# Kernel tuning notes

Measured on AMD Instinct MI355X. Metric: run time of the kernel, lower is better.

## Reference

```python
import jax, jax.numpy as jnp
import numpy as np

N_NODES = 50000
N_EDGES = 640000
WIDTH = 128
K = 5
N_CONVS = 6  # 1 input + 4 hidden + 1 output ChebConv layers


def setup_inputs() -> dict:
    key = jax.random.key(0)
    k1, k2, k3, k4 = jax.random.split(key, 4)
    scale = 1.0 / np.sqrt(WIDTH)
    x = jax.random.normal(k1, (N_NODES, WIDTH), dtype=jnp.float32)
    edge_index = jax.random.randint(k2, (2, N_EDGES), 0, N_NODES, dtype=jnp.int64)
    conv_w = jax.random.normal(k3, (N_CONVS, K, WIDTH, WIDTH), dtype=jnp.float32) * scale
    conv_b = jnp.zeros((N_CONVS, WIDTH), dtype=jnp.float32)
    lin_w = jax.random.normal(k4, (WIDTH, 1), dtype=jnp.float32) * scale
    lin_b = jnp.zeros((1,), dtype=jnp.float32)
    return {"x": x, "edge_index": edge_index, "conv_w": conv_w,
            "conv_b": conv_b, "lin_w": lin_w, "lin_b": lin_b}


def _cheb_norm(edge_index):
    # PyG ChebConv with normalization='sym', lambda_max=2.0:
    # L_hat = 2/lambda_max * (I - D^-1/2 A D^-1/2) - I = -D^-1/2 A D^-1/2
    # (diagonal terms cancel), so per-edge weight = -d_i^-1/2 * d_j^-1/2.
    src, dst = edge_index[0], edge_index[1]
    ones = jnp.ones((edge_index.shape[1],), dtype=jnp.float32)
    deg = jax.ops.segment_sum(ones, dst, num_segments=N_NODES)
    d_inv_sqrt = jnp.where(deg > 0, jax.lax.rsqrt(jnp.maximum(deg, 1e-12)), 0.0)
    return -d_inv_sqrt[src] * d_inv_sqrt[dst]


def _propagate(x, src, dst, norm):
    # L_hat @ x via gather -> weight -> scatter-add
    msg = norm[:, None] * x[src]              # [E, C]
    return jax.ops.segment_sum(msg, dst, num_segments=N_NODES)


def _cheb_conv(x, W, b, src, dst, norm):
    # Chebyshev recurrence: T0=x, T1=Lx, Tk = 2*L*T(k-1) - T(k-2)
    Tx0 = x
    out = Tx0 @ W[0]
    Tx1 = _propagate(Tx0, src, dst, norm)
    out = out + Tx1 @ W[1]
    for k in range(2, K):
        Tx2 = 2.0 * _propagate(Tx1, src, dst, norm) - Tx0
        out = out + Tx2 @ W[k]
        Tx0, Tx1 = Tx1, Tx2
    return out + b


def reference(x, edge_index, conv_w, conv_b, lin_w, lin_b):
    src, dst = edge_index[0], edge_index[1]
    norm = _cheb_norm(edge_index)
    h = x
    # first 5 convs followed by ReLU (dropout is identity in eval mode)
    for l in range(N_CONVS - 1):
        h = _cheb_conv(h, conv_w[l], conv_b[l], src, dst, norm)
        h = jax.nn.relu(h)
    # final conv (no activation) + Linear(128, 1)
    h = _cheb_conv(h, conv_w[N_CONVS - 1], conv_b[N_CONVS - 1], src, dst, norm)
    return h @ lin_w + lin_b
```

## Files before the change

kernel.cpp:

```cpp
#include <hip/hip_runtime.h>


#define NN 50000
#define NE 640000
#define WID 128

typedef __attribute__((ext_vector_type(8))) short bf16x8;
typedef __attribute__((ext_vector_type(4))) float f32x4;

__device__ __forceinline__ unsigned short f2bf(float f) {
  union { float f; unsigned int u; } v; v.f = f;
  unsigned int r = v.u + 0x7FFF + ((v.u >> 16) & 1);
  return (unsigned short)(r >> 16);
}
__device__ __forceinline__ float bflo(unsigned int u) {
  return __uint_as_float(u << 16);
}
__device__ __forceinline__ float bfhi(unsigned int u) {
  return __uint_as_float(u & 0xffff0000u);
}


__global__ __launch_bounds__(256) void degree_kernel(const int* __restrict__ ei,
                                                     int* __restrict__ deg, int E) {
  int e = blockIdx.x * 256 + threadIdx.x;
  if (e < E) atomicAdd(&deg[ei[E + e]], 1);
}

__global__ __launch_bounds__(256) void dinv_kernel(const int* __restrict__ deg,
                                                   float* __restrict__ dinv, int n) {
  int i = blockIdx.x * 256 + threadIdx.x;
  if (i < n) {
    float d = (float)deg[i];
    dinv[i] = d > 0.0f ? rsqrtf(d) : 0.0f;
  }
}

__global__ __launch_bounds__(256) void scan1_kernel(const int* __restrict__ deg,
                                                    int* __restrict__ lex,
                                                    int* __restrict__ bsum, int n) {
  __shared__ int ws[4];
  int tid = threadIdx.x, lane = tid & 63, w = tid >> 6;
  int i = blockIdx.x * 256 + tid;
  int cnt = (i < n) ? deg[i] : 0;
  int v = cnt;
#pragma unroll
  for (int off = 1; off < 64; off <<= 1) {
    int u = __shfl_up(v, off, 64);
    if (lane >= off) v += u;
  }
  if (lane == 63) ws[w] = v;
  __syncthreads();
  int wexcl = 0;
#pragma unroll
  for (int k = 0; k < 4; ++k) wexcl += (k < w) ? ws[k] : 0;
  if (i < n) lex[i] = wexcl + v - cnt;
  if (tid == 255) bsum[blockIdx.x] = wexcl + v;
}

__global__ __launch_bounds__(256) void scan2_kernel(const int* __restrict__ bsum,
                                                    int* __restrict__ boff,
                                                    int* __restrict__ row_end, int nb) {
  __shared__ int ws[4];
  int tid = threadIdx.x, lane = tid & 63, w = tid >> 6;
  int cnt = (tid < nb) ? bsum[tid] : 0;
  int v = cnt;
#pragma unroll
  for (int off = 1; off < 64; off <<= 1) {
    int u = __shfl_up(v, off, 64);
    if (lane >= off) v += u;
  }
  if (lane == 63) ws[w] = v;
  __syncthreads();
  int wexcl = 0;
#pragma unroll
  for (int k = 0; k < 4; ++k) wexcl += (k < w) ? ws[k] : 0;
  if (tid < nb) boff[tid] = wexcl + v - cnt;
  if (tid == 255) *row_end = wexcl + v;
}

__global__ __launch_bounds__(256) void scan3_kernel(const int* __restrict__ lex,
                                                    const int* __restrict__ boff,
                                                    int* __restrict__ row_start,
                                                    int* __restrict__ fill_ptr, int n) {
  int i = blockIdx.x * 256 + threadIdx.x;
  if (i < n) {
    int rs = lex[i] + boff[blockIdx.x];
    row_start[i] = rs;
    fill_ptr[i] = rs;
  }
}

__global__ __launch_bounds__(256) void fill_kernel(const int* __restrict__ ei,
                                                   const float* __restrict__ dinv,
                                                   int* __restrict__ fill_ptr,
                                                   int2* __restrict__ csr, int E) {
  int e = blockIdx.x * 256 + threadIdx.x;
  if (e < E) {
    int s = ei[e];
    int d = ei[E + e];
    int pos = atomicAdd(&fill_ptr[d], 1);
    csr[pos] = make_int2(s, __float_as_int(-dinv[s] * dinv[d]));
  }
}

__global__ __launch_bounds__(256) void cvt_x_kernel(const float* __restrict__ x,
                                                    unsigned short* __restrict__ o, int n) {
  int i = blockIdx.x * 256 + threadIdx.x;
  if (i < n) o[i] = f2bf(x[i]);
}

__global__ __launch_bounds__(256) void cvt_w_kernel(const float* __restrict__ w,
                                                    unsigned short* __restrict__ wt, int n) {
  int i = blockIdx.x * 256 + threadIdx.x;
  if (i < n) {
    int l = i / (WID * 640);
    int r = i % (WID * 640);
    int col = r / 640;
    int k = r % 640;
    int kk = k >> 7, m = k & 127;
    wt[i] = f2bf(w[(((size_t)l * 5 + kk) * WID + m) * WID + col]);
  }
}


__global__ __launch_bounds__(256) void prop_kernel(unsigned short* __restrict__ out,
                                                   const unsigned short* __restrict__ xin,
                                                   const unsigned short* __restrict__ sub,
                                                   float scale,
                                                   const int* __restrict__ row_start,
                                                   const int2* __restrict__ csr,
                                                   int n) {
  int node = blockIdx.x * 8 + (threadIdx.x >> 5);
  if (node >= n) return;
  int t = threadIdx.x & 31;
  int s = row_start[node], e = row_start[node + 1];
  float a0 = 0.f, a1 = 0.f, a2 = 0.f, a3 = 0.f;
  for (int base = s; base < e; base += 32) {
    int cnt = min(32, e - base);
    int2 ed = (t < cnt) ? csr[base + t] : make_int2(0, 0);
    int j = 0;
    for (; j + 4 <= cnt; j += 4) {
      int s0 = __shfl(ed.x, j, 32), s1 = __shfl(ed.x, j + 1, 32);
      int s2 = __shfl(ed.x, j + 2, 32), s3 = __shfl(ed.x, j + 3, 32);
      float n0 = __int_as_float(__shfl(ed.y, j, 32));
      float n1 = __int_as_float(__shfl(ed.y, j + 1, 32));
      float n2 = __int_as_float(__shfl(ed.y, j + 2, 32));
      float n3 = __int_as_float(__shfl(ed.y, j + 3, 32));
      const uint2 v0 = *(const uint2*)(xin + (size_t)s0 * WID + t * 4);
      const uint2 v1 = *(const uint2*)(xin + (size_t)s1 * WID + t * 4);
      const uint2 v2 = *(const uint2*)(xin + (size_t)s2 * WID + t * 4);
      const uint2 v3 = *(const uint2*)(xin + (size_t)s3 * WID + t * 4);
      a0 += n0 * bflo(v0.x) + n1 * bflo(v1.x) + n2 * bflo(v2.x) + n3 * bflo(v3.x);
      a1 += n0 * bfhi(v0.x) + n1 * bfhi(v1.x) + n2 * bfhi(v2.x) + n3 * bfhi(v3.x);
      a2 += n0 * bflo(v0.y) + n1 * bflo(v1.y) + n2 * bflo(v2.y) + n3 * bflo(v3.y);
      a3 += n0 * bfhi(v0.y) + n1 * bfhi(v1.y) + n2 * bfhi(v2.y) + n3 * bfhi(v3.y);
    }
    for (; j < cnt; ++j) {
      int sj = __shfl(ed.x, j, 32);
      float nj = __int_as_float(__shfl(ed.y, j, 32));
      const uint2 v = *(const uint2*)(xin + (size_t)sj * WID + t * 4);
      a0 += nj * bflo(v.x); a1 += nj * bfhi(v.x);
      a2 += nj * bflo(v.y); a3 += nj * bfhi(v.y);
    }
  }
  size_t o = (size_t)node * WID + t * 4;
  float r0 = scale * a0, r1 = scale * a1, r2 = scale * a2, r3 = scale * a3;
  if (sub) {
    const uint2 sv = *(const uint2*)(sub + o);
    r0 -= bflo(sv.x); r1 -= bfhi(sv.x);
    r2 -= bflo(sv.y); r3 -= bfhi(sv.y);
  }
  *(ushort4*)(out + o) = make_ushort4(f2bf(r0), f2bf(r1), f2bf(r2), f2bf(r3));
}


__global__ __launch_bounds__(256) void cheb_gemm(
    const unsigned short* __restrict__ T0, const unsigned short* __restrict__ T1,
    const unsigned short* __restrict__ T2, const unsigned short* __restrict__ T3,
    const unsigned short* __restrict__ T4,
    const unsigned short* __restrict__ Wt,
    const float* __restrict__ bias,
    unsigned short* __restrict__ Hb,
    const float* __restrict__ linw, const float* __restrict__ linb,
    float* __restrict__ y, int M, int mode) {
  __shared__ unsigned short As[64][40];
  __shared__ unsigned short Bs[128][40];
  const unsigned short* chunks[5] = {T0, T1, T2, T3, T4};
  int tid = threadIdx.x;
  int wave = tid >> 6, lane = tid & 63;
  int lrow = lane & 15, quad = lane >> 4;
  int rowBase = blockIdx.x * 64;

  f32x4 acc[8];
#pragma unroll
  for (int b = 0; b < 8; ++b) acc[b] = (f32x4){0.f, 0.f, 0.f, 0.f};

  int ar = tid >> 2, akof = (tid & 3) * 8;
  int agrow = min(rowBase + ar, M - 1);
  int bc = tid >> 1, bkof = (tid & 1) * 16;

  for (int kc = 0; kc < 20; ++kc) {
    const unsigned short* ch = chunks[kc >> 2];
    const unsigned short* ap = ch + (size_t)agrow * WID + (kc & 3) * 32 + akof;
    *(int4*)(&As[ar][akof]) = *(const int4*)ap;
    const unsigned short* bp = Wt + (size_t)bc * 640 + kc * 32 + bkof;
    *(int4*)(&Bs[bc][bkof]) = *(const int4*)bp;
    *(int4*)(&Bs[bc][bkof + 8]) = *(const int4*)(bp + 8);
    __syncthreads();

    bf16x8 a = *(bf16x8*)(&As[wave * 16 + lrow][quad * 8]);
#pragma unroll
    for (int ct = 0; ct < 8; ++ct) {
      bf16x8 b = *(bf16x8*)(&Bs[ct * 16 + lrow][quad * 8]);
      acc[ct] = __builtin_amdgcn_mfma_f32_16x16x32_bf16(a, b, acc[ct], 0, 0, 0);
    }
    __syncthreads();
  }

  if (mode != 2) {
#pragma unroll
    for (int ct = 0; ct < 8; ++ct) {
      int gcol = ct * 16 + lrow;
      float bv = bias[gcol];
#pragma unroll
      for (int reg = 0; reg < 4; ++reg) {
        int grow = rowBase + wave * 16 + quad * 4 + reg;
        if (grow < M) {
          float v = acc[ct][reg] + bv;
          if (mode == 1) v = fmaxf(v, 0.f);
          Hb[(size_t)grow * WID + gcol] = f2bf(v);
        }
      }
    }
  } else {
    float lwv[8], bvv[8];
#pragma unroll
    for (int ct = 0; ct < 8; ++ct) {
      int gcol = ct * 16 + lrow;
      lwv[ct] = linw[gcol];
      bvv[ct] = bias[gcol];
    }
#pragma unroll
    for (int reg = 0; reg < 4; ++reg) {
      float part = 0.f;
#pragma unroll
      for (int ct = 0; ct < 8; ++ct) part += (acc[ct][reg] + bvv[ct]) * lwv[ct];
#pragma unroll
      for (int off = 1; off < 16; off <<= 1) part += __shfl_xor(part, off, 16);
      int grow = rowBase + wave * 16 + quad * 4 + reg;
      if (lrow == 0 && grow < M) y[grow] = part + linb[0];
    }
  }
}


extern "C" void kernel_launch(void* const* d_in, const int* in_sizes, int n_in,
                              void* d_out, int out_size, void* d_ws, size_t ws_size,
                              hipStream_t stream) {
  const float* x = (const float*)d_in[0];
  const int* ei = (const int*)d_in[1];
  const float* conv_w = (const float*)d_in[2];
  const float* conv_b = (const float*)d_in[3];
  const float* lin_w = (const float*)d_in[4];
  const float* lin_b = (const float*)d_in[5];

  const int N = NN, E = NE, C = WID, L = 6;
  const int NB = (N + 255) / 256;

  char* ws = (char*)d_ws;
  size_t off = 0;
  auto alloc = [&](size_t bytes) -> void* {
    void* p = ws + off;
    off = (off + bytes + 255) & ~(size_t)255;
    return p;
  };
  int* deg = (int*)alloc((size_t)N * 4);
  float* dinv = (float*)alloc((size_t)N * 4);
  int* row_start = (int*)alloc((size_t)(N + 1) * 4);
  int* fill_ptr = (int*)alloc((size_t)N * 4);
  int* lex = (int*)alloc((size_t)N * 4);
  int* bsum = (int*)alloc((size_t)NB * 4);
  int* boff = (int*)alloc((size_t)NB * 4);
  int2* csr = (int2*)alloc((size_t)E * 8);
  unsigned short* Xbf = (unsigned short*)alloc((size_t)N * C * 2);
  unsigned short* Hb0 = (unsigned short*)alloc((size_t)N * C * 2);
  unsigned short* Hb1 = (unsigned short*)alloc((size_t)N * C * 2);
  unsigned short* T1b = (unsigned short*)alloc((size_t)N * C * 2);
  unsigned short* T2b = (unsigned short*)alloc((size_t)N * C * 2);
  unsigned short* T3b = (unsigned short*)alloc((size_t)N * C * 2);
  unsigned short* T4b = (unsigned short*)alloc((size_t)N * C * 2);
  unsigned short* Wt = (unsigned short*)alloc((size_t)L * C * 640 * 2);

  hipMemsetAsync(deg, 0, (size_t)N * 4, stream);
  degree_kernel<<<(E + 255) / 256, 256, 0, stream>>>(ei, deg, E);
  dinv_kernel<<<(N + 255) / 256, 256, 0, stream>>>(deg, dinv, N);
  scan1_kernel<<<NB, 256, 0, stream>>>(deg, lex, bsum, N);
  scan2_kernel<<<1, 256, 0, stream>>>(bsum, boff, &row_start[N], NB);
  scan3_kernel<<<NB, 256, 0, stream>>>(lex, boff, row_start, fill_ptr, N);
  fill_kernel<<<(E + 255) / 256, 256, 0, stream>>>(ei, dinv, fill_ptr, csr, E);
  cvt_x_kernel<<<(N * C + 255) / 256, 256, 0, stream>>>(x, Xbf, N * C);
  cvt_w_kernel<<<(L * C * 640 + 255) / 256, 256, 0, stream>>>(conv_w, Wt, L * C * 640);

  const int pg = (N + 7) / 8;
  const int gg = (N + 63) / 64;

  for (int l = 0; l < L; ++l) {
    const unsigned short* T0 = (l == 0) ? Xbf : ((l & 1) ? Hb0 : Hb1);
    unsigned short* Hb = (l & 1) ? Hb1 : Hb0;
    int mode = (l < L - 1) ? 1 : 2;

    prop_kernel<<<pg, 256, 0, stream>>>(T1b, T0, nullptr, 1.0f, row_start, csr, N);
    prop_kernel<<<pg, 256, 0, stream>>>(T2b, T1b, T0, 2.0f, row_start, csr, N);
    prop_kernel<<<pg, 256, 0, stream>>>(T3b, T2b, T1b, 2.0f, row_start, csr, N);
    prop_kernel<<<pg, 256, 0, stream>>>(T4b, T3b, T2b, 2.0f, row_start, csr, N);
    cheb_gemm<<<gg, 256, 0, stream>>>(T0, T1b, T2b, T3b, T4b,
                                      Wt + (size_t)l * C * 640, conv_b + (size_t)l * C,
                                      Hb, lin_w, lin_b, (float*)d_out, N, mode);
  }
}
```

Before: 972.2 us.

## Widen SpMM gather to 16-byte loads and register-prefetch GEMM tiles

The propagation kernel now assigns 16 lanes per node, each loading 8 bf16 values (uint4) per neighbor row instead of 4. This halves the shuffle and loop overhead per edge and processes twice as many nodes per block. The Chebyshev GEMM now prefetches the next K-chunk of A and B into registers while the current chunk is in shared memory, hiding global load latency behind MFMA work. The cost is more registers per thread, and the 16-lane shuffle width reduces edge-batch parallelism for high-degree nodes.

```diff
diff --git a/kernel.cpp b/kernel.cpp
--- a/kernel.cpp
+++ b/kernel.cpp
@@ -12,6 +12,9 @@
   union { float f; unsigned int u; } v; v.f = f;
   unsigned int r = v.u + 0x7FFF + ((v.u >> 16) & 1);
   return (unsigned short)(r >> 16);
+}
+__device__ __forceinline__ unsigned int pack2(float lo, float hi) {
+  return (unsigned int)f2bf(lo) | ((unsigned int)f2bf(hi) << 16);
 }
 __device__ __forceinline__ float bflo(unsigned int u) {
   return __uint_as_float(u << 16);
@@ -131,47 +134,60 @@
                                                    const int* __restrict__ row_start,
                                                    const int2* __restrict__ csr,
                                                    int n) {
-  int node = blockIdx.x * 8 + (threadIdx.x >> 5);
+  int node = blockIdx.x * 16 + (threadIdx.x >> 4);
   if (node >= n) return;
-  int t = threadIdx.x & 31;
+  int t = threadIdx.x & 15;
   int s = row_start[node], e = row_start[node + 1];
   float a0 = 0.f, a1 = 0.f, a2 = 0.f, a3 = 0.f;
-  for (int base = s; base < e; base += 32) {
-    int cnt = min(32, e - base);
+  float a4 = 0.f, a5 = 0.f, a6 = 0.f, a7 = 0.f;
+  for (int base = s; base < e; base += 16) {
+    int cnt = min(16, e - base);
     int2 ed = (t < cnt) ? csr[base + t] : make_int2(0, 0);
     int j = 0;
     for (; j + 4 <= cnt; j += 4) {
-      int s0 = __shfl(ed.x, j, 32), s1 = __shfl(ed.x, j + 1, 32);
-      int s2 = __shfl(ed.x, j + 2, 32), s3 = __shfl(ed.x, j + 3, 32);
-      float n0 = __int_as_float(__shfl(ed.y, j, 32));
-      float n1 = __int_as_float(__shfl(ed.y, j + 1, 32));
-      float n2 = __int_as_float(__shfl(ed.y, j + 2, 32));
-      float n3 = __int_as_float(__shfl(ed.y, j + 3, 32));
-      const uint2 v0 = *(const uint2*)(xin + (size_t)s0 * WID + t * 4);
-      const uint2 v1 = *(const uint2*)(xin + (size_t)s1 * WID + t * 4);
-      const uint2 v2 = *(const uint2*)(xin + (size_t)s2 * WID + t * 4);
-      const uint2 v3 = *(const uint2*)(xin + (size_t)s3 * WID + t * 4);
+      int s0 = __shfl(ed.x, j, 16), s1 = __shfl(ed.x, j + 1, 16);
+      int s2 = __shfl(ed.x, j + 2, 16), s3 = __shfl(ed.x, j + 3, 16);
+      float n0 = __int_as_float(__shfl(ed.y, j, 16));
+      float n1 = __int_as_float(__shfl(ed.y, j + 1, 16));
+      float n2 = __int_as_float(__shfl(ed.y, j + 2, 16));
+      float n3 = __int_as_float(__shfl(ed.y, j + 3, 16));
+      const uint4 v0 = *(const uint4*)(xin + (size_t)s0 * WID + t * 8);
+      const uint4 v1 = *(const uint4*)(xin + (size_t)s1 * WID + t * 8);
+      const uint4 v2 = *(const uint4*)(xin + (size_t)s2 * WID + t * 8);
+      const uint4 v3 = *(const uint4*)(xin + (size_t)s3 * WID + t * 8);
       a0 += n0 * bflo(v0.x) + n1 * bflo(v1.x) + n2 * bflo(v2.x) + n3 * bflo(v3.x);
       a1 += n0 * bfhi(v0.x) + n1 * bfhi(v1.x) + n2 * bfhi(v2.x) + n3 * bfhi(v3.x);
       a2 += n0 * bflo(v0.y) + n1 * bflo(v1.y) + n2 * bflo(v2.y) + n3 * bflo(v3.y);
       a3 += n0 * bfhi(v0.y) + n1 * bfhi(v1.y) + n2 * bfhi(v2.y) + n3 * bfhi(v3.y);
+      a4 += n0 * bflo(v0.z) + n1 * bflo(v1.z) + n2 * bflo(v2.z) + n3 * bflo(v3.z);
+      a5 += n0 * bfhi(v0.z) + n1 * bfhi(v1.z) + n2 * bfhi(v2.z) + n3 * bfhi(v3.z);
+      a6 += n0 * bflo(v0.w) + n1 * bflo(v1.w) + n2 * bflo(v2.w) + n3 * bflo(v3.w);
+      a7 += n0 * bfhi(v0.w) + n1 * bfhi(v1.w) + n2 * bfhi(v2.w) + n3 * bfhi(v3.w);
     }
     for (; j < cnt; ++j) {
-      int sj = __shfl(ed.x, j, 32);
-      float nj = __int_as_float(__shfl(ed.y, j, 32));
-      const uint2 v = *(const uint2*)(xin + (size_t)sj * WID + t * 4);
+      int sj = __shfl(ed.x, j, 16);
+      float nj = __int_as_float(__shfl(ed.y, j, 16));
+      const uint4 v = *(const uint4*)(xin + (size_t)sj * WID + t * 8);
       a0 += nj * bflo(v.x); a1 += nj * bfhi(v.x);
       a2 += nj * bflo(v.y); a3 += nj * bfhi(v.y);
-    }
-  }
-  size_t o = (size_t)node * WID + t * 4;
+      a4 += nj * bflo(v.z); a5 += nj * bfhi(v.z);
+      a6 += nj * bflo(v.w); a7 += nj * bfhi(v.w);
+    }
+  }
+  size_t o = (size_t)node * WID + t * 8;
   float r0 = scale * a0, r1 = scale * a1, r2 = scale * a2, r3 = scale * a3;
+  float r4 = scale * a4, r5 = scale * a5, r6 = scale * a6, r7 = scale * a7;
   if (sub) {
-    const uint2 sv = *(const uint2*)(sub + o);
+    const uint4 sv = *(const uint4*)(sub + o);
     r0 -= bflo(sv.x); r1 -= bfhi(sv.x);
     r2 -= bflo(sv.y); r3 -= bfhi(sv.y);
-  }
-  *(ushort4*)(out + o) = make_ushort4(f2bf(r0), f2bf(r1), f2bf(r2), f2bf(r3));
+    r4 -= bflo(sv.z); r5 -= bfhi(sv.z);
+    r6 -= bflo(sv.w); r7 -= bfhi(sv.w);
+  }
+  uint4 wv;
+  wv.x = pack2(r0, r1); wv.y = pack2(r2, r3);
+  wv.z = pack2(r4, r5); wv.w = pack2(r6, r7);
+  *(uint4*)(out + o) = wv;
 }
 
 
@@ -200,14 +216,29 @@
   int agrow = min(rowBase + ar, M - 1);
   int bc = tid >> 1, bkof = (tid & 1) * 16;
 
+  int4 aReg, bReg0, bReg1;
+  {
+    const unsigned short* ap = chunks[0] + (size_t)agrow * WID + akof;
+    aReg = *(const int4*)ap;
+    const unsigned short* bp = Wt + (size_t)bc * 640 + bkof;
+    bReg0 = *(const int4*)bp;
+    bReg1 = *(const int4*)(bp + 8);
+  }
+
   for (int kc = 0; kc < 20; ++kc) {
-    const unsigned short* ch = chunks[kc >> 2];
-    const unsigned short* ap = ch + (size_t)agrow * WID + (kc & 3) * 32 + akof;
-    *(int4*)(&As[ar][akof]) = *(const int4*)ap;
-    const unsigned short* bp = Wt + (size_t)bc * 640 + kc * 32 + bkof;
-    *(int4*)(&Bs[bc][bkof]) = *(const int4*)bp;
-    *(int4*)(&Bs[bc][bkof + 8]) = *(const int4*)(bp + 8);
+    *(int4*)(&As[ar][akof]) = aReg;
+    *(int4*)(&Bs[bc][bkof]) = bReg0;
+    *(int4*)(&Bs[bc][bkof + 8]) = bReg1;
     __syncthreads();
+
+    if (kc < 19) {
+      int kn = kc + 1;
+      const unsigned short* ap = chunks[kn >> 2] + (size_t)agrow * WID + (kn & 3) * 32 + akof;
+      aReg = *(const int4*)ap;
+      const unsigned short* bp = Wt + (size_t)bc * 640 + kn * 32 + bkof;
+      bReg0 = *(const int4*)bp;
+      bReg1 = *(const int4*)(bp + 8);
+    }
 
     bf16x8 a = *(bf16x8*)(&As[wave * 16 + lrow][quad * 8]);
 #pragma unroll
@@ -302,7 +333,7 @@
   cvt_x_kernel<<<(N * C + 255) / 256, 256, 0, stream>>>(x, Xbf, N * C);
   cvt_w_kernel<<<(L * C * 640 + 255) / 256, 256, 0, stream>>>(conv_w, Wt, L * C * 640);
 
-  const int pg = (N + 7) / 8;
+  const int pg = (N + 15) / 16;
   const int gg = (N + 63) / 64;
 
   for (int l = 0; l < L; ++l) {
```

Measured after the change: 928.5 us. -4.5%, faster.
